# Kernel tuning notes

Hardware: AMD Instinct MI355X
Metric: run time of the kernel (lower is better)

The kernel has to match this reference:

```python
import jax, jax.numpy as jnp
import numpy as np

N, F, C, H = 6144, 128, 64, 4
NEG = -1.0e10


def setup_inputs() -> dict:
    key = jax.random.key(0)
    ks = jax.random.split(key, 8)
    X = jax.random.normal(ks[0], (N, F), dtype=jnp.float32)
    A = (jax.random.uniform(ks[1], (N, N)) < 0.01).astype(jnp.float32)  # sparse-ish 0/1 adjacency
    A = A.at[jnp.arange(N), jnp.arange(N)].set(1.0)  # self loops so every row has a neighbor
    s = 1.0 / np.sqrt(F)
    W1 = jax.random.normal(ks[2], (H, F, C), dtype=jnp.float32) * s
    W2 = jax.random.normal(ks[3], (H, F, C), dtype=jnp.float32) * s
    a_self = jax.random.normal(ks[4], (H, C), dtype=jnp.float32) * (1.0 / np.sqrt(C))
    a_neigh = jax.random.normal(ks[5], (H, C), dtype=jnp.float32) * (1.0 / np.sqrt(C))
    bias = jnp.zeros((H, C), dtype=jnp.float32)
    return {"X": X, "A": A, "W1": W1, "W2": W2, "a_self": a_self, "a_neigh": a_neigh, "bias": bias}


def reference(X, A, W1, W2, a_self, a_neigh, bias):
    # Per-head projections: [H, N, C]
    feats = jnp.einsum('nf,hfc->hnc', X, W1)
    feats2 = jnp.einsum('nf,hfc->hnc', X, W2)
    # Attention logits: self term + transposed neighbor term -> [H, N, N]
    att_s = jnp.einsum('hnc,hc->hn', feats, a_self)
    att_n = jnp.einsum('hnc,hc->hn', feats, a_neigh)
    dense = att_s[:, :, None] + att_n[:, None, :]
    dense = jnp.where(dense > 0, dense, 0.2 * dense)  # LeakyReLU(0.2)
    dense = dense + NEG * (1.0 - A)[None, :, :]       # additive adjacency mask
    attn = jax.nn.softmax(dense, axis=-1)
    # Dropout layers are identity at inference.
    node = jnp.einsum('hnm,hmc->hnc', attn, feats) + feats2 + bias[:, None, :]
    out = jnp.mean(node, axis=0)  # attn_heads_reduction='average'
    return jax.nn.relu(out)
```

## Files before the change

kernel.cpp:

```cpp
#include <hip/hip_runtime.h>
#include <hip/hip_bf16.h>


#define N_NODES 6144
#define F_DIM   128
#define C_DIM   64
#define H_HEADS 4
#define HC      (H_HEADS * C_DIM)
#define MAXKW   128

typedef unsigned short u16;
typedef float v4f __attribute__((ext_vector_type(4)));

__global__ __launch_bounds__(256) void proj_kernel(
    const float* __restrict__ X,
    const float* __restrict__ W1, const float* __restrict__ W2,
    const float* __restrict__ a_self, const float* __restrict__ a_neigh,
    u16* __restrict__ featsB, float* __restrict__ feats2T,
    float* __restrict__ attsT, float* __restrict__ attnT)
{
    const int rt    = blockIdx.x;
    const int z     = blockIdx.y;
    const int h     = z >> 1;
    const int which = z & 1;

    const float* W = (which ? W2 : W1) + h * F_DIM * C_DIM;

    __shared__ float  Xs[64][132];
    __shared__ float4 Ws4[128][17];

    const int tid = threadIdx.x;

    {
        const float4* Xg = (const float4*)(X + (size_t)rt * 64 * F_DIM);
        for (int u = tid; u < 64 * 32; u += 256) {
            const int r = u >> 5, q = u & 31;
            *(float4*)&Xs[r][4 * q] = Xg[u];
        }
        const float4* Wg = (const float4*)W;
        for (int u = tid; u < 128 * 16; u += 256) {
            Ws4[u >> 4][u & 15] = Wg[u];
        }
    }
    __syncthreads();

    const int tx = tid & 15;
    const int ty = tid >> 4;

    float acc[4][4] = {};
    for (int k = 0; k < 128; k += 4) {
        const float4 b0 = Ws4[k + 0][tx];
        const float4 b1 = Ws4[k + 1][tx];
        const float4 b2 = Ws4[k + 2][tx];
        const float4 b3 = Ws4[k + 3][tx];
        #pragma unroll
        for (int i = 0; i < 4; ++i) {
            const float4 x = *(const float4*)&Xs[4 * ty + i][k];
            acc[i][0] += x.x * b0.x + x.y * b1.x + x.z * b2.x + x.w * b3.x;
            acc[i][1] += x.x * b0.y + x.y * b1.y + x.z * b2.y + x.w * b3.y;
            acc[i][2] += x.x * b0.z + x.y * b1.z + x.z * b2.z + x.w * b3.z;
            acc[i][3] += x.x * b0.w + x.y * b1.w + x.z * b2.w + x.w * b3.w;
        }
    }

    __syncthreads();
    float* Ct = &Xs[0][0];

    #pragma unroll
    for (int i = 0; i < 4; ++i) {
        const int r    = 4 * ty + i;
        const int node = rt * 64 + r;
        if (which == 0) {
            u16 p0 = __bfloat16_as_ushort(__float2bfloat16(acc[i][0]));
            u16 p1 = __bfloat16_as_ushort(__float2bfloat16(acc[i][1]));
            u16 p2 = __bfloat16_as_ushort(__float2bfloat16(acc[i][2]));
            u16 p3 = __bfloat16_as_ushort(__float2bfloat16(acc[i][3]));
            ushort4 pk; pk.x = p0; pk.y = p1; pk.z = p2; pk.w = p3;
            *(ushort4*)&featsB[(size_t)node * HC + h * C_DIM + 4 * tx] = pk;
            Ct[r * 65 + 4 * tx + 0] = acc[i][0];
            Ct[r * 65 + 4 * tx + 1] = acc[i][1];
            Ct[r * 65 + 4 * tx + 2] = acc[i][2];
            Ct[r * 65 + 4 * tx + 3] = acc[i][3];
        } else {
            *(float4*)&feats2T[(size_t)node * HC + h * C_DIM + 4 * tx] =
                make_float4(acc[i][0], acc[i][1], acc[i][2], acc[i][3]);
        }
    }

    if (which == 0) {
        __syncthreads();
        if (tid < 64) {
            const float* as_ = a_self  + h * C_DIM;
            const float* an_ = a_neigh + h * C_DIM;
            float s = 0.f, n = 0.f;
            #pragma unroll 8
            for (int c = 0; c < C_DIM; ++c) {
                const float v = Ct[tid * 65 + c];
                s += v * as_[c];
                n += v * an_[c];
            }
            const int node = rt * 64 + tid;
            attsT[node * H_HEADS + h] = s;
            attnT[node * H_HEADS + h] = n;
        }
    }
}

__global__ __launch_bounds__(256) void agg_kernel(
    const float* __restrict__ A,
    const u16* __restrict__ featsB, const float* __restrict__ feats2T,
    const float* __restrict__ attsT, const float* __restrict__ attnT,
    const float* __restrict__ bias,
    float* __restrict__ out)
{
    const int w    = threadIdx.x >> 6;
    const int lane = threadIdx.x & 63;
    const int i    = blockIdx.x * 4 + w;

    __shared__ int    idxs[4][MAXKW];
    __shared__ float4 ewsT4[4][MAXKW];
    int*    idx_w = idxs[w];
    float4* ews_w = ewsT4[w];

    const v4f* Arow = (const v4f*)(A + (size_t)i * N_NODES);
    const unsigned long long ltmask = (1ull << lane) - 1ull;
    int base = 0;
    #pragma unroll
    for (int ch = 0; ch < 4; ++ch) {
        v4f v[6];
        #pragma unroll
        for (int g = 0; g < 6; ++g)
            v[g] = __builtin_nontemporal_load(Arow + lane + 64 * (ch * 6 + g));
        #pragma unroll
        for (int g = 0; g < 6; ++g) {
            const int col = 4 * (lane + 64 * (ch * 6 + g));
            #pragma unroll
            for (int m = 0; m < 4; ++m) {
                const float x = (m == 0) ? v[g].x : (m == 1) ? v[g].y
                              : (m == 2) ? v[g].z : v[g].w;
                const bool p = (x > 0.5f);
                const unsigned long long mask = __ballot(p);
                if (p) {
                    const int pos = base + (int)__popcll(mask & ltmask);
                    if (pos < MAXKW) idx_w[pos] = col + m;
                }
                base += (int)__popcll(mask);
            }
        }
    }
    const int K = min(base, MAXKW);

    const float4 si4 = ((const float4*)attsT)[i];
    float zx = 0.f, zy = 0.f, zz = 0.f, zw = 0.f;
    #pragma unroll
    for (int r = 0; r < 2; ++r) {
        const int k = lane + 64 * r;
        if (k < K) {
            const float4 an = ((const float4*)attnT)[idx_w[k]];
            float l;
            float4 e4;
            l = si4.x + an.x; e4.x = __expf((l > 0.f) ? l : 0.2f * l);
            l = si4.y + an.y; e4.y = __expf((l > 0.f) ? l : 0.2f * l);
            l = si4.z + an.z; e4.z = __expf((l > 0.f) ? l : 0.2f * l);
            l = si4.w + an.w; e4.w = __expf((l > 0.f) ? l : 0.2f * l);
            ews_w[k] = e4;
            zx += e4.x; zy += e4.y; zz += e4.z; zw += e4.w;
        }
    }
    #pragma unroll
    for (int off = 32; off > 0; off >>= 1) {
        zx += __shfl_xor(zx, off);
        zy += __shfl_xor(zy, off);
        zz += __shfl_xor(zz, off);
        zw += __shfl_xor(zw, off);
    }
    const int hsel = lane >> 4;
    const float zinv = 1.0f / ((hsel == 0) ? zx : (hsel == 1) ? zy
                             : (hsel == 2) ? zz : zw);

    const uint2* fb = (const uint2*)featsB;
    float a0 = 0.f, a1 = 0.f, a2 = 0.f, a3 = 0.f;

    #define UPFMA(q, wgt)                                                   \
        {                                                                   \
            const float f0 = __uint_as_float((q).x << 16);                  \
            const float f1 = __uint_as_float((q).x & 0xffff0000u);          \
            const float f2 = __uint_as_float((q).y << 16);                  \
            const float f3 = __uint_as_float((q).y & 0xffff0000u);          \
            a0 += (wgt) * f0; a1 += (wgt) * f1;                             \
            a2 += (wgt) * f2; a3 += (wgt) * f3;                             \
        }

    int k = 0;
    for (; k + 8 <= K; k += 8) {
        const int4 j0 = *(const int4*)&idx_w[k];
        const int4 j1 = *(const int4*)&idx_w[k + 4];
        const float w0 = ((const float*)&ews_w[k + 0])[hsel];
        const float w1 = ((const float*)&ews_w[k + 1])[hsel];
        const float w2 = ((const float*)&ews_w[k + 2])[hsel];
        const float w3 = ((const float*)&ews_w[k + 3])[hsel];
        const float w4 = ((const float*)&ews_w[k + 4])[hsel];
        const float w5 = ((const float*)&ews_w[k + 5])[hsel];
        const float w6 = ((const float*)&ews_w[k + 6])[hsel];
        const float w7 = ((const float*)&ews_w[k + 7])[hsel];
        const uint2 q0 = fb[(size_t)j0.x * 64 + lane];
        const uint2 q1 = fb[(size_t)j0.y * 64 + lane];
        const uint2 q2 = fb[(size_t)j0.z * 64 + lane];
        const uint2 q3 = fb[(size_t)j0.w * 64 + lane];
        const uint2 q4 = fb[(size_t)j1.x * 64 + lane];
        const uint2 q5 = fb[(size_t)j1.y * 64 + lane];
        const uint2 q6 = fb[(size_t)j1.z * 64 + lane];
        const uint2 q7 = fb[(size_t)j1.w * 64 + lane];
        UPFMA(q0, w0) UPFMA(q1, w1) UPFMA(q2, w2) UPFMA(q3, w3)
        UPFMA(q4, w4) UPFMA(q5, w5) UPFMA(q6, w6) UPFMA(q7, w7)
    }
    for (; k < K; ++k) {
        const int   j  = idx_w[k];
        const float wg = ((const float*)&ews_w[k])[hsel];
        const uint2 q  = fb[(size_t)j * 64 + lane];
        UPFMA(q, wg)
    }
    #undef UPFMA

    const float4 f2 = *(const float4*)&feats2T[(size_t)i * HC + 4 * lane];
    const float4 b4 = *(const float4*)&bias[4 * lane];
    float s0 = a0 * zinv + f2.x + b4.x;
    float s1 = a1 * zinv + f2.y + b4.y;
    float s2 = a2 * zinv + f2.z + b4.z;
    float s3 = a3 * zinv + f2.w + b4.w;
    s0 += __shfl_xor(s0, 16); s0 += __shfl_xor(s0, 32);
    s1 += __shfl_xor(s1, 16); s1 += __shfl_xor(s1, 32);
    s2 += __shfl_xor(s2, 16); s2 += __shfl_xor(s2, 32);
    s3 += __shfl_xor(s3, 16); s3 += __shfl_xor(s3, 32);
    if (lane < 16) {
        float4 o;
        o.x = fmaxf(0.25f * s0, 0.f);
        o.y = fmaxf(0.25f * s1, 0.f);
        o.z = fmaxf(0.25f * s2, 0.f);
        o.w = fmaxf(0.25f * s3, 0.f);
        *(float4*)&out[(size_t)i * C_DIM + 4 * lane] = o;
    }
}

extern "C" void kernel_launch(void* const* d_in, const int* in_sizes, int n_in,
                              void* d_out, int out_size, void* d_ws, size_t ws_size,
                              hipStream_t stream) {
    const float* X       = (const float*)d_in[0];
    const float* A       = (const float*)d_in[1];
    const float* W1      = (const float*)d_in[2];
    const float* W2      = (const float*)d_in[3];
    const float* a_self  = (const float*)d_in[4];
    const float* a_neigh = (const float*)d_in[5];
    const float* bias    = (const float*)d_in[6];
    float* out = (float*)d_out;

    float* ws      = (float*)d_ws;
    float* feats2T = ws;
    float* attsT   = feats2T + (size_t)N_NODES * HC;
    float* attnT   = attsT   + (size_t)N_NODES * H_HEADS;
    u16*   featsB  = (u16*)(attnT + (size_t)N_NODES * H_HEADS);

    dim3 grid1(N_NODES / 64, H_HEADS * 2);
    proj_kernel<<<grid1, 256, 0, stream>>>(X, W1, W2, a_self, a_neigh,
                                           featsB, feats2T, attsT, attnT);

    agg_kernel<<<N_NODES / 4, 256, 0, stream>>>(A, featsB, feats2T, attsT, attnT, bias, out);
}
```

Measured before the change: 244.4 us.

## Interleave neighbor gather with adjacency scan and prefetch next A chunk

Restructures the aggregation kernel so each chunk of the adjacency row is scanned while the next chunk is prefetched into registers, and the neighbors found in a chunk are gathered and accumulated immediately. Exp weights are computed per lane for its head inline, so the separate weight pass, its shared-memory buffer and the cross-lane reduction of the softmax denominator go away. The aim is to overlap the A-row stream with the feature gathers and drop a sync-heavy phase. In exchange it uses more registers for the double buffer, recomputes exp redundantly across 16 lanes, and reads idx entries from LDS that other lanes just wrote without an explicit barrier within the wavefront.

Result: slower. 249.9 us (+2.3%).

```diff
diff --git a/kernel.cpp b/kernel.cpp
--- a/kernel.cpp
+++ b/kernel.cpp
@@ -117,27 +117,58 @@
     const int lane = threadIdx.x & 63;
     const int i    = blockIdx.x * 4 + w;
 
-    __shared__ int    idxs[4][MAXKW];
-    __shared__ float4 ewsT4[4][MAXKW];
-    int*    idx_w = idxs[w];
-    float4* ews_w = ewsT4[w];
-
+    __shared__ int idxs[4][MAXKW];
+    int* idx_w = idxs[w];
+
+    const unsigned long long ltmask = (1ull << lane) - 1ull;
     const v4f* Arow = (const v4f*)(A + (size_t)i * N_NODES);
-    const unsigned long long ltmask = (1ull << lane) - 1ull;
-    int base = 0;
+
+    const int    hsel = lane >> 4;
+    const float  si   = attsT[4 * i + hsel];
+    const float* anp  = attnT + hsel;
+    const uint2* fb   = (const uint2*)featsB;
+
+    float a0 = 0.f, a1 = 0.f, a2 = 0.f, a3 = 0.f;
+    float z  = 0.f;
+    int   base = 0;
+
+    #define UPFMA(q, e)                                                     \
+        {                                                                   \
+            a0 += (e) * __uint_as_float((q).x << 16);                       \
+            a1 += (e) * __uint_as_float((q).x & 0xffff0000u);               \
+            a2 += (e) * __uint_as_float((q).y << 16);                       \
+            a3 += (e) * __uint_as_float((q).y & 0xffff0000u);               \
+        }
+    #define EXPW(an, e)                                                     \
+        float e;                                                            \
+        {                                                                   \
+            float l = si + (an);                                            \
+            l = (l > 0.f) ? l : 0.2f * l;                                   \
+            e = __expf(l);                                                  \
+        }
+
+    v4f cur[6];
+    #pragma unroll
+    for (int g = 0; g < 6; ++g)
+        cur[g] = __builtin_nontemporal_load(Arow + lane + 64 * g);
+
     #pragma unroll
     for (int ch = 0; ch < 4; ++ch) {
-        v4f v[6];
-        #pragma unroll
-        for (int g = 0; g < 6; ++g)
-            v[g] = __builtin_nontemporal_load(Arow + lane + 64 * (ch * 6 + g));
+        v4f nxt[6];
+        if (ch < 3) {
+            #pragma unroll
+            for (int g = 0; g < 6; ++g)
+                nxt[g] = __builtin_nontemporal_load(Arow + lane + 64 * ((ch + 1) * 6 + g));
+        }
+
+        const int start = (base < MAXKW) ? base : MAXKW;
         #pragma unroll
         for (int g = 0; g < 6; ++g) {
             const int col = 4 * (lane + 64 * (ch * 6 + g));
             #pragma unroll
             for (int m = 0; m < 4; ++m) {
-                const float x = (m == 0) ? v[g].x : (m == 1) ? v[g].y
-                              : (m == 2) ? v[g].z : v[g].w;
+                const float x = (m == 0) ? cur[g].x : (m == 1) ? cur[g].y
+                              : (m == 2) ? cur[g].z : cur[g].w;
                 const bool p = (x > 0.5f);
                 const unsigned long long mask = __ballot(p);
                 if (p) {
@@ -147,81 +178,44 @@
                 base += (int)__popcll(mask);
             }
         }
-    }
-    const int K = min(base, MAXKW);
-
-    const float4 si4 = ((const float4*)attsT)[i];
-    float zx = 0.f, zy = 0.f, zz = 0.f, zw = 0.f;
-    #pragma unroll
-    for (int r = 0; r < 2; ++r) {
-        const int k = lane + 64 * r;
-        if (k < K) {
-            const float4 an = ((const float4*)attnT)[idx_w[k]];
-            float l;
-            float4 e4;
-            l = si4.x + an.x; e4.x = __expf((l > 0.f) ? l : 0.2f * l);
-            l = si4.y + an.y; e4.y = __expf((l > 0.f) ? l : 0.2f * l);
-            l = si4.z + an.z; e4.z = __expf((l > 0.f) ? l : 0.2f * l);
-            l = si4.w + an.w; e4.w = __expf((l > 0.f) ? l : 0.2f * l);
-            ews_w[k] = e4;
-            zx += e4.x; zy += e4.y; zz += e4.z; zw += e4.w;
-        }
-    }
-    #pragma unroll
-    for (int off = 32; off > 0; off >>= 1) {
-        zx += __shfl_xor(zx, off);
-        zy += __shfl_xor(zy, off);
-        zz += __shfl_xor(zz, off);
-        zw += __shfl_xor(zw, off);
-    }
-    const int hsel = lane >> 4;
-    const float zinv = 1.0f / ((hsel == 0) ? zx : (hsel == 1) ? zy
-                             : (hsel == 2) ? zz : zw);
-
-    const uint2* fb = (const uint2*)featsB;
-    float a0 = 0.f, a1 = 0.f, a2 = 0.f, a3 = 0.f;
-
-    #define UPFMA(q, wgt)                                                   \
-        {                                                                   \
-            const float f0 = __uint_as_float((q).x << 16);                  \
-            const float f1 = __uint_as_float((q).x & 0xffff0000u);          \
-            const float f2 = __uint_as_float((q).y << 16);                  \
-            const float f3 = __uint_as_float((q).y & 0xffff0000u);          \
-            a0 += (wgt) * f0; a1 += (wgt) * f1;                             \
-            a2 += (wgt) * f2; a3 += (wgt) * f3;                             \
-        }
-
-    int k = 0;
-    for (; k + 8 <= K; k += 8) {
-        const int4 j0 = *(const int4*)&idx_w[k];
-        const int4 j1 = *(const int4*)&idx_w[k + 4];
-        const float w0 = ((const float*)&ews_w[k + 0])[hsel];
-        const float w1 = ((const float*)&ews_w[k + 1])[hsel];
-        const float w2 = ((const float*)&ews_w[k + 2])[hsel];
-        const float w3 = ((const float*)&ews_w[k + 3])[hsel];
-        const float w4 = ((const float*)&ews_w[k + 4])[hsel];
-        const float w5 = ((const float*)&ews_w[k + 5])[hsel];
-        const float w6 = ((const float*)&ews_w[k + 6])[hsel];
-        const float w7 = ((const float*)&ews_w[k + 7])[hsel];
-        const uint2 q0 = fb[(size_t)j0.x * 64 + lane];
-        const uint2 q1 = fb[(size_t)j0.y * 64 + lane];
-        const uint2 q2 = fb[(size_t)j0.z * 64 + lane];
-        const uint2 q3 = fb[(size_t)j0.w * 64 + lane];
-        const uint2 q4 = fb[(size_t)j1.x * 64 + lane];
-        const uint2 q5 = fb[(size_t)j1.y * 64 + lane];
-        const uint2 q6 = fb[(size_t)j1.z * 64 + lane];
-        const uint2 q7 = fb[(size_t)j1.w * 64 + lane];
-        UPFMA(q0, w0) UPFMA(q1, w1) UPFMA(q2, w2) UPFMA(q3, w3)
-        UPFMA(q4, w4) UPFMA(q5, w5) UPFMA(q6, w6) UPFMA(q7, w7)
-    }
-    for (; k < K; ++k) {
-        const int   j  = idx_w[k];
-        const float wg = ((const float*)&ews_w[k])[hsel];
-        const uint2 q  = fb[(size_t)j * 64 + lane];
-        UPFMA(q, wg)
+        const int end = (base < MAXKW) ? base : MAXKW;
+
+        int k = start;
+        for (; k + 4 <= end; k += 4) {
+            const int j0 = idx_w[k + 0];
+            const int j1 = idx_w[k + 1];
+            const int j2 = idx_w[k + 2];
+            const int j3 = idx_w[k + 3];
+            const float an0 = anp[4 * (size_t)j0];
+            const float an1 = anp[4 * (size_t)j1];
+            const float an2 = anp[4 * (size_t)j2];
+            const float an3 = anp[4 * (size_t)j3];
+            const uint2 q0 = fb[(size_t)j0 * 64 + lane];
+            const uint2 q1 = fb[(size_t)j1 * 64 + lane];
+            const uint2 q2 = fb[(size_t)j2 * 64 + lane];
+            const uint2 q3 = fb[(size_t)j3 * 64 + lane];
+            EXPW(an0, e0) EXPW(an1, e1) EXPW(an2, e2) EXPW(an3, e3)
+            z += e0 + e1 + e2 + e3;
+            UPFMA(q0, e0) UPFMA(q1, e1) UPFMA(q2, e2) UPFMA(q3, e3)
+        }
+        for (; k < end; ++k) {
+            const int   j  = idx_w[k];
+            const float an = anp[4 * (size_t)j];
+            const uint2 q  = fb[(size_t)j * 64 + lane];
+            EXPW(an, e)
+            z += e;
+            UPFMA(q, e)
+        }
+
+        if (ch < 3) {
+            #pragma unroll
+            for (int g = 0; g < 6; ++g) cur[g] = nxt[g];
+        }
     }
     #undef UPFMA
-
+    #undef EXPW
+
+    const float zinv = 1.0f / z;
     const float4 f2 = *(const float4*)&feats2T[(size_t)i * HC + 4 * lane];
     const float4 b4 = *(const float4*)&bias[4 * lane];
     float s0 = a0 * zinv + f2.x + b4.x;
```

## Move adjacency scan into projection kernel so it overlaps projection work

Applied to the files above, without the earlier changes.

The adjacency-row scan that builds neighbor lists now runs as extra blocks inside the projection kernel instead of at the start of the aggregation kernel. Neighbor indices and counts go to workspace, and the aggregation kernel reads them back. The aim is to overlap the bandwidth-heavy scan of the 151 MB adjacency matrix with the compute-bound projection. The cost is an extra global write and read of the neighbor lists, and a shared-memory footprint in the scan blocks sized for projection, which may reduce occupancy.

Result: slower. 255.1 us (+4.4%).

```diff
diff --git a/kernel.cpp b/kernel.cpp
--- a/kernel.cpp
+++ b/kernel.cpp
@@ -9,27 +9,70 @@
 #define HC      (H_HEADS * C_DIM)
 #define MAXKW   128
 
+#define SCAN_BLOCKS (N_NODES / 4)
+#define PROJ_BLOCKS ((N_NODES / 64) * 8)
+
 typedef unsigned short u16;
 typedef float v4f __attribute__((ext_vector_type(4)));
 
-__global__ __launch_bounds__(256) void proj_kernel(
-    const float* __restrict__ X,
+__global__ __launch_bounds__(256) void scan_proj_kernel(
+    const float* __restrict__ A, const float* __restrict__ X,
     const float* __restrict__ W1, const float* __restrict__ W2,
     const float* __restrict__ a_self, const float* __restrict__ a_neigh,
     u16* __restrict__ featsB, float* __restrict__ feats2T,
-    float* __restrict__ attsT, float* __restrict__ attnT)
+    float* __restrict__ attsT, float* __restrict__ attnT,
+    int* __restrict__ nbr, int* __restrict__ nbr_cnt)
 {
-    const int rt    = blockIdx.x;
-    const int z     = blockIdx.y;
+    const int bid = blockIdx.x;
+    const int tid = threadIdx.x;
+
+    __shared__ float  Xs[64][132];
+    __shared__ float4 Ws4[128][17];
+
+    if (bid < SCAN_BLOCKS) {
+        const int w    = tid >> 6;
+        const int lane = tid & 63;
+        const int i    = bid * 4 + w;
+
+        const v4f* Arow = (const v4f*)(A + (size_t)i * N_NODES);
+        const unsigned long long ltmask = (1ull << lane) - 1ull;
+        int* nrow = nbr + (size_t)i * MAXKW;
+        int base = 0;
+
+        #pragma unroll
+        for (int ch = 0; ch < 4; ++ch) {
+            v4f v[6];
+            #pragma unroll
+            for (int g = 0; g < 6; ++g)
+                v[g] = __builtin_nontemporal_load(Arow + lane + 64 * (ch * 6 + g));
+            #pragma unroll
+            for (int g = 0; g < 6; ++g) {
+                const int col = 4 * (lane + 64 * (ch * 6 + g));
+                #pragma unroll
+                for (int m = 0; m < 4; ++m) {
+                    const float x = (m == 0) ? v[g].x : (m == 1) ? v[g].y
+                                  : (m == 2) ? v[g].z : v[g].w;
+                    const bool p = (x > 0.5f);
+                    const unsigned long long mask = __ballot(p);
+                    if (p) {
+                        const int pos = base + (int)__popcll(mask & ltmask);
+                        if (pos < MAXKW) nrow[pos] = col + m;
+                    }
+                    base += (int)__popcll(mask);
+                }
+            }
+        }
+        if (lane == 0) nbr_cnt[i] = min(base, MAXKW);
+        return;
+    }
+
+    const int p     = bid - SCAN_BLOCKS;
+    const int rt    = p % 96;
+    const int z     = p / 96;
     const int h     = z >> 1;
     const int which = z & 1;
 
     const float* W = (which ? W2 : W1) + h * F_DIM * C_DIM;
-
-    __shared__ float  Xs[64][132];
-    __shared__ float4 Ws4[128][17];
-
-    const int tid = threadIdx.x;
 
     {
         const float4* Xg = (const float4*)(X + (size_t)rt * 64 * F_DIM);
@@ -106,8 +149,8 @@
     }
 }
 
-__global__ __launch_bounds__(256) void agg_kernel(
-    const float* __restrict__ A,
+__global__ __launch_bounds__(256) void gat_kernel(
+    const int* __restrict__ nbr, const int* __restrict__ nbr_cnt,
     const u16* __restrict__ featsB, const float* __restrict__ feats2T,
     const float* __restrict__ attsT, const float* __restrict__ attnT,
     const float* __restrict__ bias,
@@ -122,33 +165,13 @@
     int*    idx_w = idxs[w];
     float4* ews_w = ewsT4[w];
 
-    const v4f* Arow = (const v4f*)(A + (size_t)i * N_NODES);
-    const unsigned long long ltmask = (1ull << lane) - 1ull;
-    int base = 0;
-    #pragma unroll
-    for (int ch = 0; ch < 4; ++ch) {
-        v4f v[6];
-        #pragma unroll
-        for (int g = 0; g < 6; ++g)
-            v[g] = __builtin_nontemporal_load(Arow + lane + 64 * (ch * 6 + g));
-        #pragma unroll
-        for (int g = 0; g < 6; ++g) {
-            const int col = 4 * (lane + 64 * (ch * 6 + g));
-            #pragma unroll
-            for (int m = 0; m < 4; ++m) {
-                const float x = (m == 0) ? v[g].x : (m == 1) ? v[g].y
-                              : (m == 2) ? v[g].z : v[g].w;
-                const bool p = (x > 0.5f);
-                const unsigned long long mask = __ballot(p);
-                if (p) {
-                    const int pos = base + (int)__popcll(mask & ltmask);
-                    if (pos < MAXKW) idx_w[pos] = col + m;
-                }
-                base += (int)__popcll(mask);
-            }
-        }
-    }
-    const int K = min(base, MAXKW);
+    const int K = nbr_cnt[i];
+    const int* nrow = nbr + (size_t)i * MAXKW;
+    #pragma unroll
+    for (int r = 0; r < 2; ++r) {
+        const int k = lane + 64 * r;
+        if (k < K) idx_w[k] = nrow[k];
+    }
 
     const float4 si4 = ((const float4*)attsT)[i];
     float zx = 0.f, zy = 0.f, zz = 0.f, zw = 0.f;
@@ -183,12 +206,10 @@
 
     #define UPFMA(q, wgt)                                                   \
         {                                                                   \
-            const float f0 = __uint_as_float((q).x << 16);                  \
-            const float f1 = __uint_as_float((q).x & 0xffff0000u);          \
-            const float f2 = __uint_as_float((q).y << 16);                  \
-            const float f3 = __uint_as_float((q).y & 0xffff0000u);          \
-            a0 += (wgt) * f0; a1 += (wgt) * f1;                             \
-            a2 += (wgt) * f2; a3 += (wgt) * f3;                             \
+            a0 += (wgt) * __uint_as_float((q).x << 16);                     \
+            a1 += (wgt) * __uint_as_float((q).x & 0xffff0000u);             \
+            a2 += (wgt) * __uint_as_float((q).y << 16);                     \
+            a3 += (wgt) * __uint_as_float((q).y & 0xffff0000u);             \
         }
 
     int k = 0;
@@ -259,10 +280,13 @@
     float* attsT   = feats2T + (size_t)N_NODES * HC;
     float* attnT   = attsT   + (size_t)N_NODES * H_HEADS;
     u16*   featsB  = (u16*)(attnT + (size_t)N_NODES * H_HEADS);
-
-    dim3 grid1(N_NODES / 64, H_HEADS * 2);
-    proj_kernel<<<grid1, 256, 0, stream>>>(X, W1, W2, a_self, a_neigh,
-                                           featsB, feats2T, attsT, attnT);
-
-    agg_kernel<<<N_NODES / 4, 256, 0, stream>>>(A, featsB, feats2T, attsT, attnT, bias, out);
+    int*   nbr     = (int*)(featsB + (size_t)N_NODES * HC);
+    int*   nbr_cnt = nbr + (size_t)N_NODES * MAXKW;
+
+    scan_proj_kernel<<<SCAN_BLOCKS + PROJ_BLOCKS, 256, 0, stream>>>(
+        A, X, W1, W2, a_self, a_neigh,
+        featsB, feats2T, attsT, attnT, nbr, nbr_cnt);
+
+    gat_kernel<<<N_NODES / 4, 256, 0, stream>>>(
+        nbr, nbr_cnt, featsB, feats2T, attsT, attnT, bias, out);
 }
```
